# Performance work log

Measured on AMD Instinct MI355X. Metric: run time of the kernel, lower is better.

The kernel has to match this reference:

```python
import jax, jax.numpy as jnp
import numpy as np

GRID = 32
N_NODES = GRID * GRID          # 1024
PATCH = 1
C_IN = 3
NODE_F = C_IN * PATCH * PATCH  # 3
HID = 256
N_CLASSES = 10


def _build_norm_adj():
    # 5-point grid stencil + self loops, symmetrically normalized: D^-1/2 A D^-1/2
    adj = np.zeros((N_NODES, N_NODES), dtype=np.float32)
    idx = np.arange(N_NODES)
    i, j = idx // GRID, idx % GRID
    adj[idx, idx] = 1.0
    for di, dj in [(-1, 0), (1, 0), (0, -1), (0, 1)]:
        ni, nj = i + di, j + dj
        ok = (ni >= 0) & (ni < GRID) & (nj >= 0) & (nj < GRID)
        adj[idx[ok], (ni * GRID + nj)[ok]] = 1.0
    deg = adj.sum(axis=1)
    dis = np.where(deg > 0, deg ** -0.5, 0.0).astype(np.float32)
    return jnp.asarray(dis[:, None] * adj * dis[None, :])


def _image_to_graph(x):
    # [B,C,H,W] -> [B, grid, patch, grid, patch] blocks -> [B, N, C*patch^2]
    B = x.shape[0]
    x = x.reshape(B, C_IN, GRID, PATCH, GRID, PATCH)
    x = jnp.transpose(x, (0, 2, 4, 1, 3, 5))
    return x.reshape(B, N_NODES, NODE_F)


def setup_inputs() -> dict:
    key = jax.random.key(0)
    ks = jax.random.split(key, 10)
    s = 0.05
    return {
        "x": jax.random.normal(ks[0], (256, 3, 32, 32), dtype=jnp.float32),
        "W1": jax.random.normal(ks[1], (HID, NODE_F), dtype=jnp.float32) * s,
        "b1": jnp.zeros((HID,), dtype=jnp.float32),
        "W2": jax.random.normal(ks[2], (HID, HID), dtype=jnp.float32) * s,
        "b2": jnp.zeros((HID,), dtype=jnp.float32),
        "W3": jax.random.normal(ks[3], (HID // 2, HID), dtype=jnp.float32) * s,
        "b3": jnp.zeros((HID // 2,), dtype=jnp.float32),
        "Wc": jax.random.normal(ks[4], (N_CLASSES, N_NODES * (HID // 2)), dtype=jnp.float32) * s,
        "bc": jnp.zeros((N_CLASSES,), dtype=jnp.float32),
        "adj": _build_norm_adj(),
    }


def _gc(h, W, b, adj):
    # Linear, then fixed-adjacency aggregation, then ReLU
    h = jnp.einsum('bnf,hf->bnh', h, W) + b
    h = jnp.einsum('mn,bnh->bmh', adj, h)
    return jax.nn.relu(h)


def reference(x, W1, b1, W2, b2, W3, b3, Wc, bc, adj):
    h = _image_to_graph(x)                 # [B, N, 3]
    h = _gc(h, W1, b1, adj)                # [B, N, 256]
    h = _gc(h, W2, b2, adj)                # [B, N, 256]
    h = _gc(h, W3, b3, adj)                # [B, N, 128]
    h = h.reshape(h.shape[0], -1)          # [B, N*128]
    return h @ Wc.T + bc                   # [B, 10]
```

## Files before the change

kernel.cpp:

```cpp
#include <hip/hip_runtime.h>
#include <stdint.h>

#define N_NODES 1024
#define NCLS 10
#define KDIM 131072

typedef unsigned short u16;
typedef __bf16 bf16x8 __attribute__((ext_vector_type(8)));
typedef float f32x4 __attribute__((ext_vector_type(4)));

__device__ __forceinline__ float b2f(u16 u) {
  union { float f; uint32_t u; } v; v.u = ((uint32_t)u) << 16; return v.f;
}
__device__ __forceinline__ float b2f_lo(uint32_t u) {
  union { float f; uint32_t u; } v; v.u = u << 16; return v.f;
}
__device__ __forceinline__ float b2f_hi(uint32_t u) {
  union { float f; uint32_t u; } v; v.u = u & 0xFFFF0000u; return v.f;
}
__device__ __forceinline__ u16 f2b(float f) {
  union { float f; uint32_t u; } v; v.f = f;
  uint32_t r = v.u + 0x7FFF + ((v.u >> 16) & 1);
  return (u16)(r >> 16);
}
__device__ __forceinline__ uint32_t pack2(float a, float b) {
  return (uint32_t)f2b(a) | ((uint32_t)f2b(b) << 16);
}

__device__ __forceinline__ void async_copy16(const u16* g, u16* l) {
  __builtin_amdgcn_global_load_lds(
      (const __attribute__((address_space(1))) void*)g,
      (__attribute__((address_space(3))) void*)l, 16, 0, 0);
}

__global__ __launch_bounds__(256) void cvt_w_kernel(const float* __restrict__ w,
                                                    u16* __restrict__ o, int n) {
  int i = blockIdx.x * 256 + threadIdx.x;
  if (i < n) o[i] = f2b(w[i]);
}

__global__ __launch_bounds__(256) void prep_wc_kernel(const float* __restrict__ wc,
                                                      u16* __restrict__ o) {
  int i = blockIdx.x * 256 + threadIdx.x;
  int row = i >> 17;
  int col = i & (KDIM - 1);
  o[i] = (row < NCLS) ? f2b(wc[row * KDIM + col]) : (u16)0;
}

__global__ __launch_bounds__(256) void prep_tab_kernel(const float* __restrict__ adj,
                                                       int* __restrict__ nbi,
                                                       float* __restrict__ nbc,
                                                       float* __restrict__ r) {
  int m = blockIdx.x * 256 + threadIdx.x;
  if (m >= N_NODES) return;
  int i = m >> 5, j = m & 31;
  const float* arow = adj + (size_t)m * N_NODES;
  int n[5]; float c[5];
  n[0] = m;                      c[0] = arow[m];
  n[1] = (i > 0)  ? m - 32 : m;  c[1] = (i > 0)  ? arow[m - 32] : 0.f;
  n[2] = (i < 31) ? m + 32 : m;  c[2] = (i < 31) ? arow[m + 32] : 0.f;
  n[3] = (j > 0)  ? m - 1  : m;  c[3] = (j > 0)  ? arow[m - 1]  : 0.f;
  n[4] = (j < 31) ? m + 1  : m;  c[4] = (j < 31) ? arow[m + 1]  : 0.f;
  float s = 0.f;
#pragma unroll
  for (int t = 0; t < 5; t++) { nbi[m * 5 + t] = n[t]; nbc[m * 5 + t] = c[t]; s += c[t]; }
  r[m] = s;
}

__global__ __launch_bounds__(256) void outinit_kernel(const float* __restrict__ bc,
                                                      float* __restrict__ out) {
  int idx = blockIdx.x * 256 + threadIdx.x;
  if (idx < 256 * NCLS) out[idx] = bc[idx % NCLS];
}

__global__ __launch_bounds__(256) void l1agg_kernel(
    const float* __restrict__ x,
    const float* __restrict__ W1,
    const float* __restrict__ b1,
    const int* __restrict__ nbi, const float* __restrict__ nbc,
    const float* __restrict__ r,
    u16* __restrict__ g)
{
  __shared__ u16 h1s[128 * 256];
  __shared__ float gxs[128][4];
  __shared__ float W1s[768];
  __shared__ float b1s[256];
  int p0 = blockIdx.x * 64;
  int b = p0 >> 10;
  int m0 = p0 & 1023;
  int e0 = m0 - 32;
  int tid = threadIdx.x;

  b1s[tid] = b1[tid];
  for (int i = tid; i < 768; i += 256) W1s[i] = W1[i];

  if (tid < 128) {
    int n = e0 + tid;
    float g0 = 0.f, g1 = 0.f, g2 = 0.f, rn = 0.f;
    if (n >= 0 && n < N_NODES) {
      const float* xb = x + (size_t)b * 3072;
#pragma unroll
      for (int t = 0; t < 5; t++) {
        int nb = nbi[n * 5 + t]; float cf = nbc[n * 5 + t];
        g0 += cf * xb[nb];
        g1 += cf * xb[1024 + nb];
        g2 += cf * xb[2048 + nb];
      }
      rn = r[n];
    }
    gxs[tid][0] = g0; gxs[tid][1] = g1; gxs[tid][2] = g2; gxs[tid][3] = rn;
  }
  __syncthreads();

  int ch8 = (tid & 31) * 8;
  float w[8][3], bb[8];
#pragma unroll
  for (int c = 0; c < 8; c++) {
    w[c][0] = W1s[(ch8 + c) * 3];
    w[c][1] = W1s[(ch8 + c) * 3 + 1];
    w[c][2] = W1s[(ch8 + c) * 3 + 2];
    bb[c] = b1s[ch8 + c];
  }

#pragma unroll
  for (int it = 0; it < 16; it++) {
    int node = (tid >> 5) + it * 8;
    float g0 = gxs[node][0], g1 = gxs[node][1], g2 = gxs[node][2], rn = gxs[node][3];
    uint32_t pk[4];
#pragma unroll
    for (int c = 0; c < 8; c += 2) {
      float z0 = fmaxf(g0 * w[c][0] + g1 * w[c][1] + g2 * w[c][2] + rn * bb[c], 0.f);
      float z1 = fmaxf(g0 * w[c+1][0] + g1 * w[c+1][1] + g2 * w[c+1][2] + rn * bb[c+1], 0.f);
      pk[c >> 1] = pack2(z0, z1);
    }
    *(uint4*)&h1s[node * 256 + ch8] = *(uint4*)pk;
  }
  __syncthreads();

#pragma unroll
  for (int it = 0; it < 8; it++) {
    int node = (tid >> 5) + it * 8;
    int m = m0 + node;
    float acc[8] = {};
#pragma unroll
    for (int t = 0; t < 5; t++) {
      int nb = nbi[m * 5 + t]; float cf = nbc[m * 5 + t];
      uint4 v = *(const uint4*)&h1s[(nb - e0) * 256 + ch8];
      acc[0] += cf * b2f_lo(v.x); acc[1] += cf * b2f_hi(v.x);
      acc[2] += cf * b2f_lo(v.y); acc[3] += cf * b2f_hi(v.y);
      acc[4] += cf * b2f_lo(v.z); acc[5] += cf * b2f_hi(v.z);
      acc[6] += cf * b2f_lo(v.w); acc[7] += cf * b2f_hi(v.w);
    }
    uint4 o;
    o.x = pack2(acc[0], acc[1]); o.y = pack2(acc[2], acc[3]);
    o.z = pack2(acc[4], acc[5]); o.w = pack2(acc[6], acc[7]);
    *(uint4*)&g[(size_t)(p0 + node) * 256 + ch8] = o;
  }
}

__global__ __launch_bounds__(256) void mm_kernel(
    const u16* __restrict__ A, const u16* __restrict__ W,
    const float* __restrict__ bias, const float* __restrict__ r,
    u16* __restrict__ C, int N)
{
  const int K = 256;
  __shared__ u16 As[128 * 64];
  __shared__ u16 Bs[128 * 64];
  int m0 = blockIdx.x * 128;
  int n0 = blockIdx.y * 128;
  int tid = threadIdx.x;
  int w = tid >> 6, l = tid & 63;
  int wm = w >> 1, wn = w & 1;

  f32x4 acc[4][4] = {};

  int r8 = l >> 3, oct = l & 7;
  int so = (oct ^ r8) << 3;
  int lrow = l & 15, lq = l >> 4;
  int o0 = (lq ^ (lrow & 7)) << 3;
  int o1 = o0 ^ 32;

  const u16* ga0 = A + (size_t)(m0 + w * 32 + r8) * K + so;
  const u16* gb0 = W + (size_t)(n0 + w * 32 + r8) * K + so;

  for (int k0 = 0; k0 < K; k0 += 64) {
#pragma unroll
    for (int q = 0; q < 4; q++) {
      async_copy16(ga0 + q * 8 * K + k0, &As[(w * 32 + q * 8) * 64]);
      async_copy16(gb0 + q * 8 * K + k0, &Bs[(w * 32 + q * 8) * 64]);
    }
    __syncthreads();

    const u16* pa = &As[(wm * 64 + lrow) * 64];
    const u16* pb = &Bs[(wn * 64 + lrow) * 64];
    bf16x8 af[4][2], bf[4][2];
#pragma unroll
    for (int t = 0; t < 4; t++) {
      af[t][0] = *(const bf16x8*)(pa + t * 16 * 64 + o0);
      af[t][1] = *(const bf16x8*)(pa + t * 16 * 64 + o1);
      bf[t][0] = *(const bf16x8*)(pb + t * 16 * 64 + o0);
      bf[t][1] = *(const bf16x8*)(pb + t * 16 * 64 + o1);
    }
#pragma unroll
    for (int kh = 0; kh < 2; kh++)
#pragma unroll
      for (int mt = 0; mt < 4; mt++)
#pragma unroll
        for (int nt = 0; nt < 4; nt++)
          acc[mt][nt] = __builtin_amdgcn_mfma_f32_16x16x32_bf16(af[mt][kh], bf[nt][kh], acc[mt][nt], 0, 0, 0);
    __syncthreads();
  }

#pragma unroll
  for (int mt = 0; mt < 4; mt++)
#pragma unroll
    for (int nt = 0; nt < 4; nt++) {
      f32x4 v = acc[mt][nt];
      int col = n0 + wn * 64 + nt * 16 + lrow;
      float bs = bias[col];
#pragma unroll
      for (int i2 = 0; i2 < 4; i2++) {
        int row = m0 + wm * 64 + mt * 16 + lq * 4 + i2;
        float val = v[i2] + r[row & 1023] * bs;
        C[(size_t)row * N + col] = f2b(fmaxf(val, 0.f));
      }
    }
}

__global__ __launch_bounds__(256) void mm3agg_kernel(
    const u16* __restrict__ H,
    const u16* __restrict__ W,
    const float* __restrict__ bias, const float* __restrict__ r,
    const int* __restrict__ nbi, const float* __restrict__ nbc,
    u16* __restrict__ C)
{
  const int K = 256, N = 128;
  const int AST = 72;
  __shared__ u16 As[128 * AST];
  __shared__ u16 Bs[128 * 64];
  int m0 = blockIdx.x * 128;
  int tid = threadIdx.x;
  int w = tid >> 6, l = tid & 63;
  int wm = w >> 1, wn = w & 1;

  f32x4 acc[4][4] = {};

  int arow = tid >> 1;
  int acol = (tid & 1) * 32;
  int pg = m0 + arow;
  int node = pg & 1023;
  const u16* hb = H + ((size_t)(pg >> 10) << 10) * 256;
  const u16* nbp[5]; float cf[5];
#pragma unroll
  for (int j = 0; j < 5; j++) {
    nbp[j] = hb + (size_t)nbi[node * 5 + j] * 256 + acol;
    cf[j] = nbc[node * 5 + j];
  }

  int r8 = l >> 3, oct = l & 7;
  int so = (oct ^ r8) << 3;
  const u16* gb0 = W + (size_t)(w * 32 + r8) * K + so;
  int lrow = l & 15, lq = l >> 4;
  int o0 = (lq ^ (lrow & 7)) << 3;
  int o1 = o0 ^ 32;

  for (int k0 = 0; k0 < K; k0 += 64) {
#pragma unroll
    for (int q = 0; q < 4; q++)
      async_copy16(gb0 + q * 8 * K + k0, &Bs[(w * 32 + q * 8) * 64]);

#pragma unroll
    for (int half = 0; half < 2; half++) {
      uint4 L[5][2];
#pragma unroll
      for (int j = 0; j < 5; j++) {
        L[j][0] = *(const uint4*)(nbp[j] + k0 + half * 16);
        L[j][1] = *(const uint4*)(nbp[j] + k0 + half * 16 + 8);
      }
      float a0[8] = {}, a1[8] = {};
#pragma unroll
      for (int j = 0; j < 5; j++) {
        float c = cf[j];
        const uint32_t* u0 = (const uint32_t*)&L[j][0];
        const uint32_t* u1 = (const uint32_t*)&L[j][1];
#pragma unroll
        for (int e = 0; e < 4; e++) {
          a0[2*e]   += c * b2f_lo(u0[e]); a0[2*e+1] += c * b2f_hi(u0[e]);
          a1[2*e]   += c * b2f_lo(u1[e]); a1[2*e+1] += c * b2f_hi(u1[e]);
        }
      }
      uint4 oa, ob;
      oa.x = pack2(a0[0], a0[1]); oa.y = pack2(a0[2], a0[3]);
      oa.z = pack2(a0[4], a0[5]); oa.w = pack2(a0[6], a0[7]);
      ob.x = pack2(a1[0], a1[1]); ob.y = pack2(a1[2], a1[3]);
      ob.z = pack2(a1[4], a1[5]); ob.w = pack2(a1[6], a1[7]);
      *(uint4*)&As[arow * AST + acol + half * 16]     = oa;
      *(uint4*)&As[arow * AST + acol + half * 16 + 8] = ob;
    }
    __syncthreads();

    const u16* pa = &As[(wm * 64 + lrow) * AST];
    const u16* pb = &Bs[(wn * 64 + lrow) * 64];
    bf16x8 af[4][2], bf[4][2];
#pragma unroll
    for (int t = 0; t < 4; t++) {
      af[t][0] = *(const bf16x8*)(pa + t * 16 * AST + lq * 8);
      af[t][1] = *(const bf16x8*)(pa + t * 16 * AST + 32 + lq * 8);
      bf[t][0] = *(const bf16x8*)(pb + t * 16 * 64 + o0);
      bf[t][1] = *(const bf16x8*)(pb + t * 16 * 64 + o1);
    }
#pragma unroll
    for (int kh = 0; kh < 2; kh++)
#pragma unroll
      for (int mt = 0; mt < 4; mt++)
#pragma unroll
        for (int nt = 0; nt < 4; nt++)
          acc[mt][nt] = __builtin_amdgcn_mfma_f32_16x16x32_bf16(af[mt][kh], bf[nt][kh], acc[mt][nt], 0, 0, 0);
    __syncthreads();
  }

#pragma unroll
  for (int mt = 0; mt < 4; mt++)
#pragma unroll
    for (int nt = 0; nt < 4; nt++) {
      f32x4 v = acc[mt][nt];
      int col = wn * 64 + nt * 16 + lrow;
      float bs = bias[col];
#pragma unroll
      for (int i2 = 0; i2 < 4; i2++) {
        int row = m0 + wm * 64 + mt * 16 + lq * 4 + i2;
        float val = v[i2] + r[row & 1023] * bs;
        C[(size_t)row * N + col] = f2b(fmaxf(val, 0.f));
      }
    }
}

__global__ __launch_bounds__(256) void cls_kernel(
    const u16* __restrict__ h3,
    const u16* __restrict__ Wcb,
    float* __restrict__ out,
    int b0)
{
  int mt = blockIdx.x;
  int split = blockIdx.y;
  int w = threadIdx.x >> 6, l = threadIdx.x & 63;
  int lrow = l & 15, lq = l >> 4;
  f32x4 acc = {};
  int kbase = split * 4096 + w * 1024;
  const u16* pa = h3 + (size_t)(mt * 16 + lrow) * KDIM + kbase + lq * 8;
  const u16* pb = Wcb + (size_t)lrow * KDIM + kbase + lq * 8;
#pragma unroll 4
  for (int kk = 0; kk < 1024; kk += 32) {
    bf16x8 a = *(const bf16x8*)(pa + kk);
    bf16x8 b = *(const bf16x8*)(pb + kk);
    acc = __builtin_amdgcn_mfma_f32_16x16x32_bf16(a, b, acc, 0, 0, 0);
  }
  if (lrow < NCLS) {
#pragma unroll
    for (int i2 = 0; i2 < 4; i2++) {
      int b = b0 + mt * 16 + lq * 4 + i2;
      atomicAdd(&out[b * NCLS + lrow], acc[i2]);
    }
  }
}

extern "C" void kernel_launch(void* const* d_in, const int* in_sizes, int n_in,
                              void* d_out, int out_size, void* d_ws, size_t ws_size,
                              hipStream_t stream) {
  const float* x   = (const float*)d_in[0];
  const float* W1  = (const float*)d_in[1];
  const float* b1  = (const float*)d_in[2];
  const float* W2  = (const float*)d_in[3];
  const float* b2  = (const float*)d_in[4];
  const float* W3  = (const float*)d_in[5];
  const float* b3  = (const float*)d_in[6];
  const float* Wc  = (const float*)d_in[7];
  const float* bc  = (const float*)d_in[8];
  const float* adj = (const float*)d_in[9];
  float* out = (float*)d_out;
  const int B = 256;

  uint8_t* ws = (uint8_t*)d_ws;
  u16* W2b = (u16*)ws;  ws += (size_t)256 * 256 * 2;
  u16* W3b = (u16*)ws;  ws += (size_t)128 * 256 * 2;
  u16* Wcb = (u16*)ws;  ws += (size_t)16 * KDIM * 2;
  float* rr  = (float*)ws; ws += 1024 * 4;
  int*   nbi = (int*)ws;   ws += 1024 * 5 * 4;
  float* nbc = (float*)ws; ws += 1024 * 5 * 4;
  uintptr_t al = ((uintptr_t)ws + 255) & ~(uintptr_t)255;
  ws = (uint8_t*)al;
  size_t used = (size_t)(ws - (uint8_t*)d_ws);
  size_t avail = (ws_size > used) ? ws_size - used : 0;
  int chunk = 256;
  while (chunk > 32 && (size_t)chunk * 1024 * 256 * 2 * 2 > avail) chunk >>= 1;
  u16* bufA = (u16*)ws;
  u16* bufB = bufA + (size_t)chunk * 1024 * 256;

  cvt_w_kernel<<<256, 256, 0, stream>>>(W2, W2b, 256 * 256);
  cvt_w_kernel<<<128, 256, 0, stream>>>(W3, W3b, 128 * 256);
  prep_wc_kernel<<<(16 * KDIM) / 256, 256, 0, stream>>>(Wc, Wcb);
  prep_tab_kernel<<<4, 256, 0, stream>>>(adj, nbi, nbc, rr);
  outinit_kernel<<<(256 * NCLS + 255) / 256, 256, 0, stream>>>(bc, out);

  for (int b0 = 0; b0 < B; b0 += chunk) {
    const float* xb = x + (size_t)b0 * 3 * 1024;
    int M = chunk * 1024;
    l1agg_kernel<<<M / 64, 256, 0, stream>>>(xb, W1, b1, nbi, nbc, rr, bufB);
    {
      dim3 g(M / 128, 2);
      mm_kernel<<<g, 256, 0, stream>>>(bufB, W2b, b2, rr, bufA, 256);
    }
    mm3agg_kernel<<<M / 128, 256, 0, stream>>>(bufA, W3b, b3, rr, nbi, nbc, bufB);
    dim3 gc(chunk / 16, 32);
    cls_kernel<<<gc, 256, 0, stream>>>(bufB, Wcb, out, b0);
  }
}
```

Measured before the change: 378.8 us.

## Stage full K in LDS for GEMMs, single sync, packed bf16 convert

mm_kernel and mm3agg_kernel now load the whole K=256 slice of A and B into LDS up front, with one barrier instead of per-k-step load/sync loops. mm3agg computes the full aggregated A row tile before any MFMA runs. The mm_kernel grid is transposed so that the two N-tiles sharing an A tile run in adjacent blocks, which should improve L2 reuse. Float-to-bf16 packing uses the hardware cvt_pk builtin when it is available. The larger LDS footprint (128KB in mm_kernel, about 130KB in mm3agg) cuts occupancy to one block per CU and removes overlap of loads with compute inside a block.

Measured after the change: 430.0 us. +13.5%, slower.

```diff
diff --git a/kernel.cpp b/kernel.cpp
--- a/kernel.cpp
+++ b/kernel.cpp
@@ -9,9 +9,6 @@
 typedef __bf16 bf16x8 __attribute__((ext_vector_type(8)));
 typedef float f32x4 __attribute__((ext_vector_type(4)));
 
-__device__ __forceinline__ float b2f(u16 u) {
-  union { float f; uint32_t u; } v; v.u = ((uint32_t)u) << 16; return v.f;
-}
 __device__ __forceinline__ float b2f_lo(uint32_t u) {
   union { float f; uint32_t u; } v; v.u = u << 16; return v.f;
 }
@@ -23,14 +20,33 @@
   uint32_t r = v.u + 0x7FFF + ((v.u >> 16) & 1);
   return (u16)(r >> 16);
 }
-__device__ __forceinline__ uint32_t pack2(float a, float b) {
-  return (uint32_t)f2b(a) | ((uint32_t)f2b(b) << 16);
+__device__ __forceinline__ uint32_t pkbf(float a, float b) {
+#if __has_builtin(__builtin_amdgcn_cvt_pk_bf16_f32)
+  typedef __bf16 bf2 __attribute__((ext_vector_type(2)));
+  bf2 r = __builtin_amdgcn_cvt_pk_bf16_f32(a, b);
+  union { bf2 v; uint32_t u; } c; c.v = r; return c.u;
+#else
+  union { float f; uint32_t u; } va, vb; va.f = a; vb.f = b;
+  uint32_t ra = (va.u + 0x7FFF + ((va.u >> 16) & 1)) >> 16;
+  uint32_t rb = (vb.u + 0x7FFF + ((vb.u >> 16) & 1)) & 0xFFFF0000u;
+  return ra | rb;
+#endif
 }
 
 __device__ __forceinline__ void async_copy16(const u16* g, u16* l) {
   __builtin_amdgcn_global_load_lds(
       (const __attribute__((address_space(1))) void*)g,
       (__attribute__((address_space(3))) void*)l, 16, 0, 0);
+}
+
+__device__ __forceinline__ void agg8(const u16* p, float c, float2* acc) {
+  uint4 v = *(const uint4*)p;
+  const uint32_t* u = (const uint32_t*)&v;
+#pragma unroll
+  for (int e = 0; e < 4; e++) {
+    acc[e].x += c * b2f_lo(u[e]);
+    acc[e].y += c * b2f_hi(u[e]);
+  }
 }
 
 __global__ __launch_bounds__(256) void cvt_w_kernel(const float* __restrict__ w,
@@ -131,7 +147,7 @@
     for (int c = 0; c < 8; c += 2) {
       float z0 = fmaxf(g0 * w[c][0] + g1 * w[c][1] + g2 * w[c][2] + rn * bb[c], 0.f);
       float z1 = fmaxf(g0 * w[c+1][0] + g1 * w[c+1][1] + g2 * w[c+1][2] + rn * bb[c+1], 0.f);
-      pk[c >> 1] = pack2(z0, z1);
+      pk[c >> 1] = pkbf(z0, z1);
     }
     *(uint4*)&h1s[node * 256 + ch8] = *(uint4*)pk;
   }
@@ -141,19 +157,15 @@
   for (int it = 0; it < 8; it++) {
     int node = (tid >> 5) + it * 8;
     int m = m0 + node;
-    float acc[8] = {};
+    float2 acc[4] = {};
 #pragma unroll
     for (int t = 0; t < 5; t++) {
       int nb = nbi[m * 5 + t]; float cf = nbc[m * 5 + t];
-      uint4 v = *(const uint4*)&h1s[(nb - e0) * 256 + ch8];
-      acc[0] += cf * b2f_lo(v.x); acc[1] += cf * b2f_hi(v.x);
-      acc[2] += cf * b2f_lo(v.y); acc[3] += cf * b2f_hi(v.y);
-      acc[4] += cf * b2f_lo(v.z); acc[5] += cf * b2f_hi(v.z);
-      acc[6] += cf * b2f_lo(v.w); acc[7] += cf * b2f_hi(v.w);
+      agg8(&h1s[(nb - e0) * 256 + ch8], cf, acc);
     }
     uint4 o;
-    o.x = pack2(acc[0], acc[1]); o.y = pack2(acc[2], acc[3]);
-    o.z = pack2(acc[4], acc[5]); o.w = pack2(acc[6], acc[7]);
+    o.x = pkbf(acc[0].x, acc[0].y); o.y = pkbf(acc[1].x, acc[1].y);
+    o.z = pkbf(acc[2].x, acc[2].y); o.w = pkbf(acc[3].x, acc[3].y);
     *(uint4*)&g[(size_t)(p0 + node) * 256 + ch8] = o;
   }
 }
@@ -164,51 +176,47 @@
     u16* __restrict__ C, int N)
 {
   const int K = 256;
-  __shared__ u16 As[128 * 64];
-  __shared__ u16 Bs[128 * 64];
-  int m0 = blockIdx.x * 128;
-  int n0 = blockIdx.y * 128;
+  __shared__ u16 As[4 * 128 * 64];
+  __shared__ u16 Bs[4 * 128 * 64];
+  int n0 = blockIdx.x * 128;
+  int m0 = blockIdx.y * 128;
   int tid = threadIdx.x;
   int w = tid >> 6, l = tid & 63;
   int wm = w >> 1, wn = w & 1;
 
-  f32x4 acc[4][4] = {};
-
   int r8 = l >> 3, oct = l & 7;
   int so = (oct ^ r8) << 3;
-  int lrow = l & 15, lq = l >> 4;
-  int o0 = (lq ^ (lrow & 7)) << 3;
-  int o1 = o0 ^ 32;
-
   const u16* ga0 = A + (size_t)(m0 + w * 32 + r8) * K + so;
   const u16* gb0 = W + (size_t)(n0 + w * 32 + r8) * K + so;
 
-  for (int k0 = 0; k0 < K; k0 += 64) {
+#pragma unroll
+  for (int kg = 0; kg < 4; kg++)
 #pragma unroll
     for (int q = 0; q < 4; q++) {
-      async_copy16(ga0 + q * 8 * K + k0, &As[(w * 32 + q * 8) * 64]);
-      async_copy16(gb0 + q * 8 * K + k0, &Bs[(w * 32 + q * 8) * 64]);
-    }
-    __syncthreads();
-
-    const u16* pa = &As[(wm * 64 + lrow) * 64];
-    const u16* pb = &Bs[(wn * 64 + lrow) * 64];
-    bf16x8 af[4][2], bf[4][2];
+      async_copy16(ga0 + (size_t)q * 8 * K + kg * 64, &As[kg * 8192 + (w * 32 + q * 8) * 64]);
+      async_copy16(gb0 + (size_t)q * 8 * K + kg * 64, &Bs[kg * 8192 + (w * 32 + q * 8) * 64]);
+    }
+
+  f32x4 acc[4][4] = {};
+  int lrow = l & 15, lq = l >> 4;
+  int s = lrow & 7;
+  __syncthreads();
+
+#pragma unroll
+  for (int kq = 0; kq < 8; kq++) {
+    int kg = kq >> 1, kh = kq & 1;
+    int po = (((kh << 2) | lq) ^ s) << 3;
+    bf16x8 af[4], bf[4];
 #pragma unroll
     for (int t = 0; t < 4; t++) {
-      af[t][0] = *(const bf16x8*)(pa + t * 16 * 64 + o0);
-      af[t][1] = *(const bf16x8*)(pa + t * 16 * 64 + o1);
-      bf[t][0] = *(const bf16x8*)(pb + t * 16 * 64 + o0);
-      bf[t][1] = *(const bf16x8*)(pb + t * 16 * 64 + o1);
-    }
-#pragma unroll
-    for (int kh = 0; kh < 2; kh++)
-#pragma unroll
-      for (int mt = 0; mt < 4; mt++)
-#pragma unroll
-        for (int nt = 0; nt < 4; nt++)
-          acc[mt][nt] = __builtin_amdgcn_mfma_f32_16x16x32_bf16(af[mt][kh], bf[nt][kh], acc[mt][nt], 0, 0, 0);
-    __syncthreads();
+      af[t] = *(const bf16x8*)(&As[kg * 8192 + (wm * 64 + t * 16 + lrow) * 64 + po]);
+      bf[t] = *(const bf16x8*)(&Bs[kg * 8192 + (wn * 64 + t * 16 + lrow) * 64 + po]);
+    }
+#pragma unroll
+    for (int mt = 0; mt < 4; mt++)
+#pragma unroll
+      for (int nt = 0; nt < 4; nt++)
+        acc[mt][nt] = __builtin_amdgcn_mfma_f32_16x16x32_bf16(af[mt], bf[nt], acc[mt][nt], 0, 0, 0);
   }
 
 #pragma unroll
@@ -235,88 +243,69 @@
     u16* __restrict__ C)
 {
   const int K = 256, N = 128;
-  const int AST = 72;
+  const int AST = 264;
   __shared__ u16 As[128 * AST];
-  __shared__ u16 Bs[128 * 64];
+  __shared__ u16 Bs[4 * 128 * 64];
   int m0 = blockIdx.x * 128;
   int tid = threadIdx.x;
   int w = tid >> 6, l = tid & 63;
   int wm = w >> 1, wn = w & 1;
 
-  f32x4 acc[4][4] = {};
-
-  int arow = tid >> 1;
-  int acol = (tid & 1) * 32;
-  int pg = m0 + arow;
-  int node = pg & 1023;
-  const u16* hb = H + ((size_t)(pg >> 10) << 10) * 256;
-  const u16* nbp[5]; float cf[5];
-#pragma unroll
-  for (int j = 0; j < 5; j++) {
-    nbp[j] = hb + (size_t)nbi[node * 5 + j] * 256 + acol;
-    cf[j] = nbc[node * 5 + j];
-  }
-
   int r8 = l >> 3, oct = l & 7;
   int so = (oct ^ r8) << 3;
   const u16* gb0 = W + (size_t)(w * 32 + r8) * K + so;
+#pragma unroll
+  for (int kg = 0; kg < 4; kg++)
+#pragma unroll
+    for (int q = 0; q < 4; q++)
+      async_copy16(gb0 + (size_t)q * 8 * K + kg * 64, &Bs[kg * 8192 + (w * 32 + q * 8) * 64]);
+
+  {
+    int arow = tid >> 1;
+    int acol0 = (tid & 1) * 128;
+    int pg = m0 + arow;
+    int node = pg & 1023;
+    const u16* hb = H + ((size_t)(pg >> 10) << 10) * 256 + acol0;
+    const u16* nbp[5]; float cf[5];
+#pragma unroll
+    for (int j = 0; j < 5; j++) {
+      nbp[j] = hb + (size_t)nbi[node * 5 + j] * 256;
+      cf[j] = nbc[node * 5 + j];
+    }
+    u16* dst = &As[arow * AST + acol0];
+#pragma unroll 4
+    for (int u = 0; u < 16; u++) {
+      float2 acc[4] = {};
+#pragma unroll
+      for (int j = 0; j < 5; j++) agg8(nbp[j] + u * 8, cf[j], acc);
+      uint4 o;
+      o.x = pkbf(acc[0].x, acc[0].y); o.y = pkbf(acc[1].x, acc[1].y);
+      o.z = pkbf(acc[2].x, acc[2].y); o.w = pkbf(acc[3].x, acc[3].y);
+      *(uint4*)(dst + u * 8) = o;
+    }
+  }
+
+  f32x4 acc[4][4] = {};
   int lrow = l & 15, lq = l >> 4;
-  int o0 = (lq ^ (lrow & 7)) << 3;
-  int o1 = o0 ^ 32;
-
-  for (int k0 = 0; k0 < K; k0 += 64) {
-#pragma unroll
-    for (int q = 0; q < 4; q++)
-      async_copy16(gb0 + q * 8 * K + k0, &Bs[(w * 32 + q * 8) * 64]);
-
-#pragma unroll
-    for (int half = 0; half < 2; half++) {
-      uint4 L[5][2];
-#pragma unroll
-      for (int j = 0; j < 5; j++) {
-        L[j][0] = *(const uint4*)(nbp[j] + k0 + half * 16);
-        L[j][1] = *(const uint4*)(nbp[j] + k0 + half * 16 + 8);
-      }
-      float a0[8] = {}, a1[8] = {};
-#pragma unroll
-      for (int j = 0; j < 5; j++) {
-        float c = cf[j];
-        const uint32_t* u0 = (const uint32_t*)&L[j][0];
-        const uint32_t* u1 = (const uint32_t*)&L[j][1];
-#pragma unroll
-        for (int e = 0; e < 4; e++) {
-          a0[2*e]   += c * b2f_lo(u0[e]); a0[2*e+1] += c * b2f_hi(u0[e]);
-          a1[2*e]   += c * b2f_lo(u1[e]); a1[2*e+1] += c * b2f_hi(u1[e]);
-        }
-      }
-      uint4 oa, ob;
-      oa.x = pack2(a0[0], a0[1]); oa.y = pack2(a0[2], a0[3]);
-      oa.z = pack2(a0[4], a0[5]); oa.w = pack2(a0[6], a0[7]);
-      ob.x = pack2(a1[0], a1[1]); ob.y = pack2(a1[2], a1[3]);
-      ob.z = pack2(a1[4], a1[5]); ob.w = pack2(a1[6], a1[7]);
-      *(uint4*)&As[arow * AST + acol + half * 16]     = oa;
-      *(uint4*)&As[arow * AST + acol + half * 16 + 8] = ob;
-    }
-    __syncthreads();
-
-    const u16* pa = &As[(wm * 64 + lrow) * AST];
-    const u16* pb = &Bs[(wn * 64 + lrow) * 64];
-    bf16x8 af[4][2], bf[4][2];
+  int s = lrow & 7;
+  __syncthreads();
+
+  const u16* pa = &As[(wm * 64 + lrow) * AST];
+#pragma unroll
+  for (int kq = 0; kq < 8; kq++) {
+    int kg = kq >> 1, kh = kq & 1;
+    int po = (((kh << 2) | lq) ^ s) << 3;
+    bf16x8 af[4], bf[4];
 #pragma unroll
     for (int t = 0; t < 4; t++) {
-      af[t][0] = *(const bf16x8*)(pa + t * 16 * AST + lq * 8);
-      af[t][1] = *(const bf16x8*)(pa + t * 16 * AST + 32 + lq * 8);
-      bf[t][0] = *(const bf16x8*)(pb + t * 16 * 64 + o0);
-      bf[t][1] = *(const bf16x8*)(pb + t * 16 * 64 + o1);
-    }
-#pragma unroll
-    for (int kh = 0; kh < 2; kh++)
-#pragma unroll
-      for (int mt = 0; mt < 4; mt++)
-#pragma unroll
-        for (int nt = 0; nt < 4; nt++)
-          acc[mt][nt] = __builtin_amdgcn_mfma_f32_16x16x32_bf16(af[mt][kh], bf[nt][kh], acc[mt][nt], 0, 0, 0);
-    __syncthreads();
+      af[t] = *(const bf16x8*)(pa + t * 16 * AST + kq * 32 + lq * 8);
+      bf[t] = *(const bf16x8*)(&Bs[kg * 8192 + (wn * 64 + t * 16 + lrow) * 64 + po]);
+    }
+#pragma unroll
+    for (int mt = 0; mt < 4; mt++)
+#pragma unroll
+      for (int nt = 0; nt < 4; nt++)
+        acc[mt][nt] = __builtin_amdgcn_mfma_f32_16x16x32_bf16(af[mt], bf[nt], acc[mt][nt], 0, 0, 0);
   }
 
 #pragma unroll
@@ -407,7 +396,7 @@
     int M = chunk * 1024;
     l1agg_kernel<<<M / 64, 256, 0, stream>>>(xb, W1, b1, nbi, nbc, rr, bufB);
     {
-      dim3 g(M / 128, 2);
+      dim3 g(2, M / 128);
       mm_kernel<<<g, 256, 0, stream>>>(bufB, W2b, b2, rr, bufA, 256);
     }
     mm3agg_kernel<<<M / 128, 256, 0, stream>>>(bufA, W3b, b3, rr, nbi, nbc, bufB);
```
